# Kernel optimization log

Measured on AMD Instinct MI355X. Metric: run time of the kernel, lower is better.

The kernel has to match this reference:

```python
import jax, jax.numpy as jnp
import numpy as np

B, S, H, V = 4, 2048, 768, 32000
HID = 100          # self.hidden_size
N_LABELS = 3
LN2 = 0.6931471805599453


def setup_inputs() -> dict:
    key = jax.random.key(0)
    ks = jax.random.split(key, 10)
    return {
        "input_ids": jax.random.randint(ks[0], (B, S), 0, V),
        "attention_mask": jnp.ones((B, S), jnp.float32),
        "sentiment": jax.random.normal(ks[1], (B, 3), jnp.float32),
        "hidden_states": jax.random.normal(ks[2], (B, S, H), jnp.float32),
        "lm_logits": jax.random.normal(ks[3], (B, S, V), jnp.float32),
        "W_ih": jax.random.normal(ks[4], (4 * HID, H + 1), jnp.float32) * 0.05,
        "W_hh": jax.random.normal(ks[5], (4 * HID, HID), jnp.float32) * 0.05,
        "b_ih": jax.random.normal(ks[6], (4 * HID,), jnp.float32) * 0.05,
        "b_hh": jax.random.normal(ks[7], (4 * HID,), jnp.float32) * 0.05,
        "cls_W": jax.random.normal(ks[8], (N_LABELS, HID + 3), jnp.float32) * 0.05,
        "cls_b": jax.random.normal(ks[9], (N_LABELS,), jnp.float32) * 0.05,
    }


def _lstm_last(x, W_ih, W_hh, b_ih, b_hh):
    # x: [B,S,D] -> last hidden state [B,HID]; PyTorch gate order i,f,g,o
    b, hid = x.shape[0], W_hh.shape[1]
    x_proj = jnp.einsum('bsd,gd->bsg', x, W_ih) + b_ih + b_hh  # [B,S,4H]

    def step(carry, xt):
        h, c = carry
        gates = xt + h @ W_hh.T
        i, f, g, o = jnp.split(gates, 4, axis=-1)
        c = jax.nn.sigmoid(f) * c + jax.nn.sigmoid(i) * jnp.tanh(g)
        h = jax.nn.sigmoid(o) * jnp.tanh(c)
        return (h, c), None

    h0 = jnp.zeros((b, hid), x.dtype)
    (hT, _), _ = jax.lax.scan(step, (h0, h0), jnp.swapaxes(x_proj, 0, 1))
    return hT


def reference(input_ids, attention_mask, sentiment, hidden_states, lm_logits,
              W_ih, W_hh, b_ih, b_hh, cls_W, cls_b):
    # surprisal: -log2(softmax(logits)[input_ids]) * mask, detached
    log_p = jax.nn.log_softmax(lm_logits, axis=-1)                       # [B,S,V]
    lp = jnp.take_along_axis(log_p, input_ids[..., None], axis=2)[..., 0]  # [B,S]
    surp = jax.lax.stop_gradient((-lp / LN2) * attention_mask)

    x = jnp.concatenate([hidden_states, surp[..., None]], axis=-1)  # [B,S,H+1]
    hT = _lstm_last(x, W_ih, W_hh, b_ih, b_hh)                      # [B,HID]
    # dropout is identity at inference
    feat = jnp.concatenate([hT, sentiment], axis=1)                 # [B,HID+3]
    return feat @ cls_W.T + cls_b                                   # [B,N_LABELS]
```

## Files before the change

kernel.cpp:

```cpp
#include <hip/hip_runtime.h>
#include <hip/hip_bf16.h>
#include <math.h>

#define B 4
#define S 2048
#define H 768
#define V 32000
#define HID 100
#define G4 400
#define M_TOT (B*S)
#define PD 4

typedef _Float16 half2_t __attribute__((ext_vector_type(2)));
typedef _Float16 half8_t __attribute__((ext_vector_type(8)));

__device__ __forceinline__ float fdot2_(half2_t a, half2_t b, float c) {
#if __has_builtin(__builtin_amdgcn_fdot2)
  return __builtin_amdgcn_fdot2(a, b, c, false);
#else
  return c + (float)a[0] * (float)b[0] + (float)a[1] * (float)b[1];
#endif
}

__device__ __forceinline__ float sigmoidf_(float x) {
  return 1.0f / (1.0f + __expf(-x));
}
__device__ __forceinline__ float tanhf_(float x) {
  float ax = fabsf(x);
  float e = __expf(-2.0f * ax);
  float t = (1.0f - e) / (1.0f + e);
  return copysignf(t, x);
}

__device__ __forceinline__ void lds_barrier_() {
  asm volatile("s_waitcnt lgkmcnt(0)" ::: "memory");
  __builtin_amdgcn_s_barrier();
  asm volatile("" ::: "memory");
}

__global__ __launch_bounds__(256) void surprisal_kernel(
    const float* __restrict__ logits, const int* __restrict__ ids,
    const float* __restrict__ mask, float* __restrict__ surp) {
  int row = blockIdx.x;
  const float* x = logits + (size_t)row * V;
  int tid = threadIdx.x;
  float m = -INFINITY, s = 0.0f;
  const float4* x4 = (const float4*)x;
  for (int i = tid; i < V / 4; i += 256) {
    float4 v = x4[i];
    float mv = fmaxf(fmaxf(v.x, v.y), fmaxf(v.z, v.w));
    if (mv > m) { s *= __expf(m - mv); m = mv; }
    s += __expf(v.x - m) + __expf(v.y - m) + __expf(v.z - m) + __expf(v.w - m);
  }
  #pragma unroll
  for (int off = 32; off > 0; off >>= 1) {
    float mo = __shfl_xor(m, off);
    float so = __shfl_xor(s, off);
    float mn = fmaxf(m, mo);
    s = s * __expf(m - mn) + so * __expf(mo - mn);
    m = mn;
  }
  __shared__ float sm[4], ss[4];
  int wid = tid >> 6, lane = tid & 63;
  if (lane == 0) { sm[wid] = m; ss[wid] = s; }
  __syncthreads();
  if (tid == 0) {
    float M = sm[0], Ssum = ss[0];
    #pragma unroll
    for (int w = 1; w < 4; ++w) {
      float mo = sm[w], so = ss[w];
      float mn = fmaxf(M, mo);
      Ssum = Ssum * __expf(M - mn) + so * __expf(mo - mn);
      M = mn;
    }
    float xid = x[ids[row]];
    surp[row] = (M + __logf(Ssum) - xid) * 1.4426950408889634f * mask[row];
  }
}

#define BM 64
#define BN 64
#define BK 32

__global__ __launch_bounds__(256) void xproj_kernel(
    const float* __restrict__ A,
    const float* __restrict__ surp,
    const float* __restrict__ W,
    const float* __restrict__ b_ih, const float* __restrict__ b_hh,
    float* __restrict__ xproj) {
  __shared__ float As[BK][BM];
  __shared__ float Bs[BK][BN];
  int tid = threadIdx.x;
  int m0 = blockIdx.x * BM;
  int n0 = blockIdx.y * BN;
  int tx = tid & 15, ty = tid >> 4;
  float acc[4][4] = {};
  for (int k0 = 0; k0 < H; k0 += BK) {
    #pragma unroll
    for (int l = 0; l < 2; ++l) {
      int idx = tid + l * 256;
      int row = idx >> 3;
      int kq = idx & 7;
      float4 v = *(const float4*)&A[(size_t)(m0 + row) * H + k0 + kq * 4];
      As[kq * 4 + 0][row] = v.x;
      As[kq * 4 + 1][row] = v.y;
      As[kq * 4 + 2][row] = v.z;
      As[kq * 4 + 3][row] = v.w;
    }
    #pragma unroll
    for (int l = 0; l < 8; ++l) {
      int idx = tid + l * 256;
      int n = idx >> 5;
      int kk = idx & 31;
      int gn = n0 + n;
      Bs[kk][n] = (gn < G4) ? W[(size_t)gn * (H + 1) + k0 + kk] : 0.0f;
    }
    __syncthreads();
    #pragma unroll
    for (int k = 0; k < BK; ++k) {
      float4 a = *(const float4*)&As[k][ty * 4];
      float4 bq = *(const float4*)&Bs[k][tx * 4];
      float av[4] = {a.x, a.y, a.z, a.w};
      float bv[4] = {bq.x, bq.y, bq.z, bq.w};
      #pragma unroll
      for (int i = 0; i < 4; ++i)
        #pragma unroll
        for (int j = 0; j < 4; ++j)
          acc[i][j] += av[i] * bv[j];
    }
    __syncthreads();
  }
  #pragma unroll
  for (int i = 0; i < 4; ++i) {
    int gm = m0 + ty * 4 + i;
    float sv = surp[gm];
    #pragma unroll
    for (int j = 0; j < 4; ++j) {
      int gn = n0 + tx * 4 + j;
      if (gn < G4) {
        float val = acc[i][j] + sv * W[(size_t)gn * (H + 1) + H] + b_ih[gn] + b_hh[gn];
        xproj[(size_t)gm * G4 + gn] = val;
      }
    }
  }
}

#define NH2 52
__global__ __launch_bounds__(256, 1) void lstm_kernel(
    const float* __restrict__ xproj,
    const float* __restrict__ W_hh,
    const float* __restrict__ sent,
    const float* __restrict__ cls_W,
    const float* __restrict__ cls_b,
    float* __restrict__ out) {
  int b = blockIdx.x;
  int tid = threadIdx.x;
  __shared__ __align__(16) _Float16 h_s[2 * NH2];
  __shared__ float gates_s[G4];

  bool active = tid < 200;
  int r0 = 2 * tid, r1 = 2 * tid + 1;

  half2_t w0[NH2], w1[NH2];
  if (active) {
    const float* wr0 = W_hh + (size_t)r0 * HID;
    const float* wr1 = W_hh + (size_t)r1 * HID;
    #pragma unroll
    for (int j = 0; j < 50; ++j) {
      w0[j] = half2_t{(_Float16)wr0[2 * j], (_Float16)wr0[2 * j + 1]};
      w1[j] = half2_t{(_Float16)wr1[2 * j], (_Float16)wr1[2 * j + 1]};
    }
  }
  #pragma unroll
  for (int j = 50; j < NH2; ++j) { w0[j] = half2_t{0, 0}; w1[j] = half2_t{0, 0}; }

  float c_reg = 0.0f;
  if (tid < 2 * NH2) h_s[tid] = (_Float16)0;
  __syncthreads();

  const float* xp = xproj + (size_t)b * S * G4;
  float2 xr[PD];
  #pragma unroll
  for (int d = 0; d < PD; ++d)
    xr[d] = active ? ((const float2*)(xp + (size_t)d * G4))[tid] : float2{0.f, 0.f};

  #pragma unroll 4
  for (int t = 0; t < S; ++t) {
    int slot = t & (PD - 1);

    if (active) {
      float a0 = 0.f, a1 = 0.f, b0 = 0.f, b1 = 0.f;
      const half8_t* h8 = (const half8_t*)h_s;
      #pragma unroll
      for (int j = 0; j < 13; ++j) {
        half8_t hv = h8[j];
        half2_t ha = {hv[0], hv[1]}, hb = {hv[2], hv[3]};
        half2_t hc = {hv[4], hv[5]}, hd = {hv[6], hv[7]};
        a0 = fdot2_(w0[4 * j + 0], ha, a0);
        a1 = fdot2_(w1[4 * j + 0], ha, a1);
        a0 = fdot2_(w0[4 * j + 1], hb, a0);
        a1 = fdot2_(w1[4 * j + 1], hb, a1);
        a0 = fdot2_(w0[4 * j + 2], hc, a0);
        a1 = fdot2_(w1[4 * j + 2], hc, a1);
        a0 = fdot2_(w0[4 * j + 3], hd, a0);
        a1 = fdot2_(w1[4 * j + 3], hd, a1);
      }
      *(float2*)&gates_s[r0] = float2{a0 + xr[slot].x, a1 + xr[slot].y};
    }

    {
      int tp = (t + PD < S) ? (t + PD) : (S - 1);
      xr[slot] = active ? ((const float2*)(xp + (size_t)tp * G4))[tid]
                        : float2{0.f, 0.f};
    }

    lds_barrier_();

    if (tid < HID) {
      float ig = sigmoidf_(gates_s[tid]);
      float fg = sigmoidf_(gates_s[HID + tid]);
      float gg = tanhf_(gates_s[2 * HID + tid]);
      float og = sigmoidf_(gates_s[3 * HID + tid]);
      c_reg = fg * c_reg + ig * gg;
      h_s[tid] = (_Float16)(og * tanhf_(c_reg));
    }

    lds_barrier_();
  }

  if (tid < 3) {
    float acc = cls_b[tid];
    const float* cw = cls_W + tid * (HID + 3);
    #pragma unroll
    for (int j = 0; j < HID; ++j) acc += cw[j] * (float)h_s[j];
    #pragma unroll
    for (int k2 = 0; k2 < 3; ++k2) acc += cw[HID + k2] * sent[b * 3 + k2];
    out[b * 3 + tid] = acc;
  }
}

extern "C" void kernel_launch(void* const* d_in, const int* in_sizes, int n_in,
                              void* d_out, int out_size, void* d_ws, size_t ws_size,
                              hipStream_t stream) {
  const int*   input_ids = (const int*)d_in[0];
  const float* mask      = (const float*)d_in[1];
  const float* sent      = (const float*)d_in[2];
  const float* hs        = (const float*)d_in[3];
  const float* logits    = (const float*)d_in[4];
  const float* W_ih      = (const float*)d_in[5];
  const float* W_hh      = (const float*)d_in[6];
  const float* b_ih      = (const float*)d_in[7];
  const float* b_hh      = (const float*)d_in[8];
  const float* cls_W     = (const float*)d_in[9];
  const float* cls_b     = (const float*)d_in[10];
  float* out = (float*)d_out;

  float* surp  = (float*)d_ws;
  float* xproj = surp + M_TOT;

  surprisal_kernel<<<M_TOT, 256, 0, stream>>>(logits, input_ids, mask, surp);
  xproj_kernel<<<dim3(M_TOT / BM, (G4 + BN - 1) / BN), 256, 0, stream>>>(
      hs, surp, W_ih, b_ih, b_hh, xproj);
  lstm_kernel<<<B, 256, 0, stream>>>(xproj, W_hh, sent, cls_W, cls_b, out);
}
```

Baseline: 1.719 ms.

## Compute all four gates per hidden unit in one thread to drop a barrier

The recurrent LSTM kernel is restructured so each of 100 threads holds the four W_hh rows for its hidden unit and computes the i, f, g and o gates itself. This removes the shared-memory gate buffer and one block barrier per time step. The hidden state is double-buffered in LDS, so a single barrier per step is enough. In exchange each thread does twice the dot-product work per step and holds more weight registers, with the block shrunk to 128 threads and prefetch depth reduced to 2.

```diff
diff --git a/kernel.cpp b/kernel.cpp
--- a/kernel.cpp
+++ b/kernel.cpp
@@ -9,7 +9,7 @@
 #define HID 100
 #define G4 400
 #define M_TOT (B*S)
-#define PD 4
+#define PD 2
 
 typedef _Float16 half2_t __attribute__((ext_vector_type(2)));
 typedef _Float16 half8_t __attribute__((ext_vector_type(8)));
@@ -146,7 +146,7 @@
 }
 
 #define NH2 52
-__global__ __launch_bounds__(256, 1) void lstm_kernel(
+__global__ __launch_bounds__(128, 1) void lstm_kernel(
     const float* __restrict__ xproj,
     const float* __restrict__ W_hh,
     const float* __restrict__ sent,
@@ -155,75 +155,98 @@
     float* __restrict__ out) {
   int b = blockIdx.x;
   int tid = threadIdx.x;
-  __shared__ __align__(16) _Float16 h_s[2 * NH2];
-  __shared__ float gates_s[G4];
-
-  bool active = tid < 200;
-  int r0 = 2 * tid, r1 = 2 * tid + 1;
-
-  half2_t w0[NH2], w1[NH2];
-  if (active) {
-    const float* wr0 = W_hh + (size_t)r0 * HID;
-    const float* wr1 = W_hh + (size_t)r1 * HID;
+  __shared__ __align__(16) _Float16 hb0[2 * NH2];
+  __shared__ __align__(16) _Float16 hb1[2 * NH2];
+
+  bool active = tid < HID;
+  int u = active ? tid : (HID - 1);
+
+  half2_t wi[NH2], wf[NH2], wg[NH2], wo[NH2];
+  {
+    const float* pi = W_hh + (size_t)u * HID;
+    const float* pf = W_hh + (size_t)(HID + u) * HID;
+    const float* pg = W_hh + (size_t)(2 * HID + u) * HID;
+    const float* po = W_hh + (size_t)(3 * HID + u) * HID;
     #pragma unroll
     for (int j = 0; j < 50; ++j) {
-      w0[j] = half2_t{(_Float16)wr0[2 * j], (_Float16)wr0[2 * j + 1]};
-      w1[j] = half2_t{(_Float16)wr1[2 * j], (_Float16)wr1[2 * j + 1]};
-    }
-  }
+      wi[j] = half2_t{(_Float16)pi[2 * j], (_Float16)pi[2 * j + 1]};
+      wf[j] = half2_t{(_Float16)pf[2 * j], (_Float16)pf[2 * j + 1]};
+      wg[j] = half2_t{(_Float16)pg[2 * j], (_Float16)pg[2 * j + 1]};
+      wo[j] = half2_t{(_Float16)po[2 * j], (_Float16)po[2 * j + 1]};
+    }
+    #pragma unroll
+    for (int j = 50; j < NH2; ++j) {
+      wi[j] = half2_t{0, 0}; wf[j] = half2_t{0, 0};
+      wg[j] = half2_t{0, 0}; wo[j] = half2_t{0, 0};
+    }
+  }
+
+  float c_reg = 0.0f;
+  if (tid < 2 * NH2) { hb0[tid] = (_Float16)0; hb1[tid] = (_Float16)0; }
+  __syncthreads();
+
+  const float* xp = xproj + (size_t)b * S * G4;
+  float xi[PD], xf[PD], xg[PD], xo[PD];
   #pragma unroll
-  for (int j = 50; j < NH2; ++j) { w0[j] = half2_t{0, 0}; w1[j] = half2_t{0, 0}; }
-
-  float c_reg = 0.0f;
-  if (tid < 2 * NH2) h_s[tid] = (_Float16)0;
-  __syncthreads();
-
-  const float* xp = xproj + (size_t)b * S * G4;
-  float2 xr[PD];
-  #pragma unroll
-  for (int d = 0; d < PD; ++d)
-    xr[d] = active ? ((const float2*)(xp + (size_t)d * G4))[tid] : float2{0.f, 0.f};
-
-  #pragma unroll 4
+  for (int d = 0; d < PD; ++d) {
+    const float* p = xp + (size_t)d * G4;
+    xi[d] = p[u];
+    xf[d] = p[HID + u];
+    xg[d] = p[2 * HID + u];
+    xo[d] = p[3 * HID + u];
+  }
+
+  #pragma unroll 2
   for (int t = 0; t < S; ++t) {
     int slot = t & (PD - 1);
-
-    if (active) {
-      float a0 = 0.f, a1 = 0.f, b0 = 0.f, b1 = 0.f;
-      const half8_t* h8 = (const half8_t*)h_s;
-      #pragma unroll
-      for (int j = 0; j < 13; ++j) {
-        half8_t hv = h8[j];
-        half2_t ha = {hv[0], hv[1]}, hb = {hv[2], hv[3]};
-        half2_t hc = {hv[4], hv[5]}, hd = {hv[6], hv[7]};
-        a0 = fdot2_(w0[4 * j + 0], ha, a0);
-        a1 = fdot2_(w1[4 * j + 0], ha, a1);
-        a0 = fdot2_(w0[4 * j + 1], hb, a0);
-        a1 = fdot2_(w1[4 * j + 1], hb, a1);
-        a0 = fdot2_(w0[4 * j + 2], hc, a0);
-        a1 = fdot2_(w1[4 * j + 2], hc, a1);
-        a0 = fdot2_(w0[4 * j + 3], hd, a0);
-        a1 = fdot2_(w1[4 * j + 3], hd, a1);
-      }
-      *(float2*)&gates_s[r0] = float2{a0 + xr[slot].x, a1 + xr[slot].y};
-    }
+    const half8_t* hr = (t & 1) ? (const half8_t*)hb0 : (const half8_t*)hb1;
+    _Float16* hw = (t & 1) ? hb1 : hb0;
+
+    float i0 = 0.f, i1 = 0.f, f0 = 0.f, f1 = 0.f;
+    float g0 = 0.f, g1 = 0.f, o0 = 0.f, o1 = 0.f;
+    #pragma unroll
+    for (int j = 0; j < 13; ++j) {
+      half8_t hv = hr[j];
+      half2_t h0 = {hv[0], hv[1]}, h1 = {hv[2], hv[3]};
+      half2_t h2 = {hv[4], hv[5]}, h3 = {hv[6], hv[7]};
+      i0 = fdot2_(wi[4 * j + 0], h0, i0);
+      f0 = fdot2_(wf[4 * j + 0], h0, f0);
+      g0 = fdot2_(wg[4 * j + 0], h0, g0);
+      o0 = fdot2_(wo[4 * j + 0], h0, o0);
+      i1 = fdot2_(wi[4 * j + 1], h1, i1);
+      f1 = fdot2_(wf[4 * j + 1], h1, f1);
+      g1 = fdot2_(wg[4 * j + 1], h1, g1);
+      o1 = fdot2_(wo[4 * j + 1], h1, o1);
+      i0 = fdot2_(wi[4 * j + 2], h2, i0);
+      f0 = fdot2_(wf[4 * j + 2], h2, f0);
+      g0 = fdot2_(wg[4 * j + 2], h2, g0);
+      o0 = fdot2_(wo[4 * j + 2], h2, o0);
+      i1 = fdot2_(wi[4 * j + 3], h3, i1);
+      f1 = fdot2_(wf[4 * j + 3], h3, f1);
+      g1 = fdot2_(wg[4 * j + 3], h3, g1);
+      o1 = fdot2_(wo[4 * j + 3], h3, o1);
+    }
+    float ai = i0 + i1 + xi[slot];
+    float af = f0 + f1 + xf[slot];
+    float ag = g0 + g1 + xg[slot];
+    float ao = o0 + o1 + xo[slot];
 
     {
       int tp = (t + PD < S) ? (t + PD) : (S - 1);
-      xr[slot] = active ? ((const float2*)(xp + (size_t)tp * G4))[tid]
-                        : float2{0.f, 0.f};
-    }
-
-    lds_barrier_();
-
-    if (tid < HID) {
-      float ig = sigmoidf_(gates_s[tid]);
-      float fg = sigmoidf_(gates_s[HID + tid]);
-      float gg = tanhf_(gates_s[2 * HID + tid]);
-      float og = sigmoidf_(gates_s[3 * HID + tid]);
-      c_reg = fg * c_reg + ig * gg;
-      h_s[tid] = (_Float16)(og * tanhf_(c_reg));
-    }
+      const float* p = xp + (size_t)tp * G4;
+      xi[slot] = p[u];
+      xf[slot] = p[HID + u];
+      xg[slot] = p[2 * HID + u];
+      xo[slot] = p[3 * HID + u];
+    }
+
+    float ig = sigmoidf_(ai);
+    float fg = sigmoidf_(af);
+    float gg = tanhf_(ag);
+    float og = sigmoidf_(ao);
+    c_reg = fg * c_reg + ig * gg;
+    float h = og * tanhf_(c_reg);
+    if (active) hw[tid] = (_Float16)h;
 
     lds_barrier_();
   }
@@ -232,7 +255,7 @@
     float acc = cls_b[tid];
     const float* cw = cls_W + tid * (HID + 3);
     #pragma unroll
-    for (int j = 0; j < HID; ++j) acc += cw[j] * (float)h_s[j];
+    for (int j = 0; j < HID; ++j) acc += cw[j] * (float)hb1[j];
     #pragma unroll
     for (int k2 = 0; k2 < 3; ++k2) acc += cw[HID + k2] * sent[b * 3 + k2];
     out[b * 3 + tid] = acc;
@@ -261,5 +284,5 @@
   surprisal_kernel<<<M_TOT, 256, 0, stream>>>(logits, input_ids, mask, surp);
   xproj_kernel<<<dim3(M_TOT / BM, (G4 + BN - 1) / BN), 256, 0, stream>>>(
       hs, surp, W_ih, b_ih, b_hh, xproj);
-  lstm_kernel<<<B, 256, 0, stream>>>(xproj, W_hh, sent, cls_W, cls_b, out);
-}
+  lstm_kernel<<<B, 128, 0, stream>>>(xproj, W_hh, sent, cls_W, cls_b, out);
+}
```

Result: slower. 1.950 ms (+13.4%).
